# Optimization experiments

Measured on AMD Instinct MI355X. Metric: run time of the kernel, lower is better.

## Reference

```python
import jax, jax.numpy as jnp
import numpy as np

N = 50000      # nodes
E = 800000     # edges in normalized A (incl. self loops)
DIN = 128      # input_dim
DOUT = 64      # output_dim
BN_EPS = 1e-5
SLOPE = 0.01   # LeakyReLU default negative slope


def setup_inputs() -> dict:
    key = jax.random.key(0)
    ks = jax.random.split(key, 10)
    H = jax.random.normal(ks[0], (N, DIN), dtype=jnp.float32)
    rows = jax.random.randint(ks[1], (E,), 0, N, dtype=jnp.int32)
    cols = jax.random.randint(ks[2], (E,), 0, N, dtype=jnp.int32)
    # values of the symmetrically normalized adjacency (precomputed in __init__)
    vals = jax.random.uniform(ks[3], (E,), dtype=jnp.float32)
    # BatchNorm1d params/buffers (eval mode: use running stats)
    gamma = 1.0 + 0.1 * jax.random.normal(ks[4], (DIN,), dtype=jnp.float32)
    beta = 0.1 * jax.random.normal(ks[5], (DIN,), dtype=jnp.float32)
    run_mean = 0.1 * jax.random.normal(ks[6], (DIN,), dtype=jnp.float32)
    run_var = 0.5 + jax.random.uniform(ks[7], (DIN,), dtype=jnp.float32)
    # Linear(input_dim, output_dim)
    W = jax.random.normal(ks[8], (DIN, DOUT), dtype=jnp.float32) / np.sqrt(DIN)
    b = 0.01 * jax.random.normal(ks[9], (DOUT,), dtype=jnp.float32)
    return dict(H=H, rows=rows, cols=cols, vals=vals, gamma=gamma, beta=beta,
                run_mean=run_mean, run_var=run_var, W=W, b=b)


def reference(H, rows, cols, vals, gamma, beta, run_mean, run_var, W, b):
    # F.normalize: L2 row normalization with eps=1e-12
    norm = jnp.maximum(jnp.linalg.norm(H, axis=1, keepdims=True), 1e-12)
    Hn = H / norm
    # BatchNorm1d (eval: running stats); dropout is identity in eval
    scale = gamma * jax.lax.rsqrt(run_var + BN_EPS)
    Hb = (Hn - run_mean) * scale + beta
    # Linear projection [N, DIN] @ [DIN, DOUT]
    X = Hb @ W + b
    # SpMM: out[r] = sum_{e: rows[e]==r} vals[e] * X[cols[e]]
    msgs = vals[:, None] * X[cols]            # [E, DOUT] gather + scale
    out = jax.ops.segment_sum(msgs, rows, num_segments=N)
    # LeakyReLU
    return jnp.where(out >= 0, out, SLOPE * out)
```

## Files before the change

kernel.cpp:

```cpp
#include <hip/hip_runtime.h>
#include <hip/hip_fp16.h>

#define N_NODES 50000
#define E_EDGES 800000
#define DIN 128
#define DOUT 64
#define NBUK 196
#define BUKCAP 4608
#define CHUNK 2048
#define NBLKA 391
#define KXBLK 782
#define ASTRIDE 136

typedef short short8 __attribute__((ext_vector_type(8)));
typedef float f32x4 __attribute__((ext_vector_type(4)));

static __device__ __forceinline__ short f2bf(float f)
{
    union { float f; unsigned u; } x{f};
    const unsigned r = x.u + 0x7FFFu + ((x.u >> 16) & 1u);
    return (short)(r >> 16);
}

union SMemFront {
    struct { short A[64][ASTRIDE]; short B[64][ASTRIDE]; } x;
    struct {
        int lhist[NBUK]; int lstart[NBUK]; int lcur[NBUK]; int gbase[NBUK];
        int scn[256];
        unsigned lbinVC[CHUNK];
        unsigned short lbinBR[CHUNK];
    } a;
};

__global__ __launch_bounds__(256) void k_front(
    const float* __restrict__ H, const float* __restrict__ gamma,
    const float* __restrict__ beta, const float* __restrict__ mean,
    const float* __restrict__ var, const float* __restrict__ W,
    const float* __restrict__ bias, unsigned short* __restrict__ X16,
    const int* __restrict__ rows, const int* __restrict__ cols,
    const float* __restrict__ vals, int* __restrict__ gcursor,
    unsigned* __restrict__ midVC, unsigned char* __restrict__ midR)
{
    __shared__ SMemFront sm;
    const int t = threadIdx.x;

    if (blockIdx.x < NBLKA) {
        const int e0 = blockIdx.x * CHUNK;
        const int nC = min(CHUNK, E_EDGES - e0);

        if (t < NBUK) sm.a.lhist[t] = 0;
        __syncthreads();

        unsigned prVC[8];
        unsigned short prBR[8];
#pragma unroll
        for (int k = 0; k < 8; ++k) {
            const int e = e0 + k * 256 + t;
            if (e < E_EDGES) {
                const int r = rows[e];
                const unsigned hv = __half_as_ushort(__float2half(vals[e]));
                prVC[k] = (hv << 16) | (unsigned)cols[e];
                prBR[k] = (unsigned short)r;
                atomicAdd(&sm.a.lhist[r >> 8], 1);
            } else {
                prBR[k] = 0xFFFFu;
            }
        }
        __syncthreads();

        const int v = (t < NBUK) ? sm.a.lhist[t] : 0;
        sm.a.scn[t] = v;
        __syncthreads();
        for (int o = 1; o < 256; o <<= 1) {
            int u = 0;
            if (t >= o) u = sm.a.scn[t - o];
            __syncthreads();
            sm.a.scn[t] += u;
            __syncthreads();
        }
        if (t < NBUK) {
            const int ex = sm.a.scn[t] - v;
            sm.a.lstart[t] = ex;
            sm.a.lcur[t] = ex;
            sm.a.gbase[t] = t * BUKCAP + (v ? atomicAdd(&gcursor[t], v) : 0);
        }
        __syncthreads();

#pragma unroll
        for (int k = 0; k < 8; ++k) {
            if (prBR[k] != 0xFFFFu) {
                const int bk = prBR[k] >> 8;
                const int pos = atomicAdd(&sm.a.lcur[bk], 1);
                sm.a.lbinVC[pos] = prVC[k];
                sm.a.lbinBR[pos] = prBR[k];
            }
        }
        __syncthreads();

        for (int i = t; i < nC; i += 256) {
            const unsigned short br = sm.a.lbinBR[i];
            const int bk = br >> 8;
            const int g = sm.a.gbase[bk] + (i - sm.a.lstart[bk]);
            if (g < (bk + 1) * BUKCAP) {
                midVC[g] = sm.a.lbinVC[i];
                midR[g] = (unsigned char)(br & 255);
            }
        }
        return;
    }

    const int l = t & 63, wv = t >> 6;
    const int R0 = (blockIdx.x - NBLKA) * 64;

    {
        const int n = t >> 2, koff = (t & 3) * 32;
#pragma unroll
        for (int i = 0; i < 16; ++i) {
            const int k = koff + i * 2;
            const unsigned lo = (unsigned short)f2bf(W[k * DOUT + n]);
            const unsigned hi = (unsigned short)f2bf(W[(k + 1) * DOUT + n]);
            *(unsigned*)&sm.x.B[n][k] = lo | (hi << 16);
        }
    }
    {
        const int rloc = t >> 2, sub = t & 3;
        const int r = R0 + rloc;
        float4 h[8];
        if (r < N_NODES) {
            const float4* hp = (const float4*)(H + (size_t)r * DIN + sub * 32);
#pragma unroll
            for (int i = 0; i < 8; ++i) h[i] = hp[i];
        } else {
#pragma unroll
            for (int i = 0; i < 8; ++i) h[i] = make_float4(0.f, 0.f, 0.f, 0.f);
        }
        float ss = 0.f;
#pragma unroll
        for (int i = 0; i < 8; ++i)
            ss += h[i].x * h[i].x + h[i].y * h[i].y + h[i].z * h[i].z + h[i].w * h[i].w;
        ss += __shfl_xor(ss, 1, 64);
        ss += __shfl_xor(ss, 2, 64);
        const float inv = 1.0f / fmaxf(sqrtf(ss), 1e-12f);

        const float4* gp = (const float4*)(gamma + sub * 32);
        const float4* bp = (const float4*)(beta  + sub * 32);
        const float4* mp = (const float4*)(mean  + sub * 32);
        const float4* vp = (const float4*)(var   + sub * 32);
#pragma unroll
        for (int i = 0; i < 8; ++i) {
            const float4 g4 = gp[i], b4 = bp[i], m4 = mp[i], v4 = vp[i];
            const float s0 = g4.x * rsqrtf(v4.x + 1e-5f);
            const float s1 = g4.y * rsqrtf(v4.y + 1e-5f);
            const float s2 = g4.z * rsqrtf(v4.z + 1e-5f);
            const float s3 = g4.w * rsqrtf(v4.w + 1e-5f);
            const float e0 = h[i].x * inv * s0 + (b4.x - m4.x * s0);
            const float e1 = h[i].y * inv * s1 + (b4.y - m4.y * s1);
            const float e2 = h[i].z * inv * s2 + (b4.z - m4.z * s2);
            const float e3 = h[i].w * inv * s3 + (b4.w - m4.w * s3);
            const unsigned u0 = (unsigned short)f2bf(e0) | ((unsigned)(unsigned short)f2bf(e1) << 16);
            const unsigned u1 = (unsigned short)f2bf(e2) | ((unsigned)(unsigned short)f2bf(e3) << 16);
            *(uint2*)&sm.x.A[rloc][sub * 32 + i * 4] = make_uint2(u0, u1);
        }
    }

    const int ml = l & 15, q = l >> 4;
    f32x4 c0, c1, c2, c3;
    {
        const float b0 = bias[ml],      b1 = bias[16 + ml];
        const float b2 = bias[32 + ml], b3 = bias[48 + ml];
        c0 = f32x4{b0, b0, b0, b0};
        c1 = f32x4{b1, b1, b1, b1};
        c2 = f32x4{b2, b2, b2, b2};
        c3 = f32x4{b3, b3, b3, b3};
    }
    __syncthreads();

#pragma unroll
    for (int k0 = 0; k0 < 4; ++k0) {
        const short8 a  = *(const short8*)&sm.x.A[wv * 16 + ml][k0 * 32 + q * 8];
        const short8 b0 = *(const short8*)&sm.x.B[ml][k0 * 32 + q * 8];
        const short8 b1 = *(const short8*)&sm.x.B[16 + ml][k0 * 32 + q * 8];
        const short8 b2 = *(const short8*)&sm.x.B[32 + ml][k0 * 32 + q * 8];
        const short8 b3 = *(const short8*)&sm.x.B[48 + ml][k0 * 32 + q * 8];
        c0 = __builtin_amdgcn_mfma_f32_16x16x32_bf16(a, b0, c0, 0, 0, 0);
        c1 = __builtin_amdgcn_mfma_f32_16x16x32_bf16(a, b1, c1, 0, 0, 0);
        c2 = __builtin_amdgcn_mfma_f32_16x16x32_bf16(a, b2, c2, 0, 0, 0);
        c3 = __builtin_amdgcn_mfma_f32_16x16x32_bf16(a, b3, c3, 0, 0, 0);
    }

    __syncthreads();
    unsigned short* otile = (unsigned short*)&sm.x.A[0][0];
#pragma unroll
    for (int i = 0; i < 4; ++i) {
        const int r = wv * 16 + q * 4 + i;
        otile[r * 64 + ml]      = __half_as_ushort(__float2half(c0[i]));
        otile[r * 64 + 16 + ml] = __half_as_ushort(__float2half(c1[i]));
        otile[r * 64 + 32 + ml] = __half_as_ushort(__float2half(c2[i]));
        otile[r * 64 + 48 + ml] = __half_as_ushort(__float2half(c3[i]));
    }
    __syncthreads();
#pragma unroll
    for (int rep = 0; rep < 2; ++rep) {
        const int id = rep * 256 + t;
        const int row = id >> 3;
        const int off = (id & 7) * 8;
        if (R0 + row < N_NODES)
            *(uint4*)(X16 + (size_t)(R0 + row) * DOUT + off) =
                *(const uint4*)&otile[row * 64 + off];
    }
}

__global__ __launch_bounds__(512) void k_passB(
    const int* __restrict__ gcursor, const unsigned* __restrict__ midVC,
    const unsigned char* __restrict__ midR, unsigned* __restrict__ ev,
    int* __restrict__ rowS, int* __restrict__ rowE)
{
    __shared__ int lhist[256], scn[256], lcur[256];
    const int t = threadIdx.x;
    const int b = blockIdx.x;
    const int base = b * BUKCAP;
    const int total = min(gcursor[b], BUKCAP);

    if (t < 256) lhist[t] = 0;
    __syncthreads();
    for (int i = t; i < total; i += 512)
        atomicAdd(&lhist[midR[base + i]], 1);
    __syncthreads();

    const int v = (t < 256) ? lhist[t] : 0;
    if (t < 256) scn[t] = v;
    __syncthreads();
    for (int o = 1; o < 256; o <<= 1) {
        int u = 0;
        if (t < 256 && t >= o) u = scn[t - o];
        __syncthreads();
        if (t < 256) scn[t] += u;
        __syncthreads();
    }
    if (t < 256) {
        const int ex = scn[t] - v;
        lcur[t] = ex;
        const int gr = (b << 8) | t;
        if (gr < N_NODES) { rowS[gr] = base + ex; rowE[gr] = base + ex + v; }
    }
    __syncthreads();

    for (int i = t; i < total; i += 512) {
        const int lr = midR[base + i];
        const int pos = atomicAdd(&lcur[lr], 1);
        ev[base + pos] = midVC[base + i];
    }
}

__global__ __launch_bounds__(256) void k_spmm(
    const int* __restrict__ rowS, const int* __restrict__ rowE,
    const unsigned* __restrict__ ev, const unsigned short* __restrict__ X16,
    float* __restrict__ out)
{
    const int lane = threadIdx.x & 63;
    const int sub  = lane & 15;
    const int g4   = lane >> 4;
    const int row  = blockIdx.x * 4 + (threadIdx.x >> 6);
    const int s  = rowS[row];
    const int e2 = rowE[row];
    float a0 = 0.f, a1 = 0.f, a2 = 0.f, a3 = 0.f;
    for (int c = s; c < e2; c += 64) {
        const int idx = c + lane;
        unsigned p = 0;
        if (idx < e2) p = ev[idx];
        const int cnt  = min(e2 - c, 64);
        const int jmax = (cnt + 3) >> 2;
        int j = 0;
        for (; j + 1 < jmax; j += 2) {
            const unsigned u0 = (unsigned)__shfl((int)p, j * 4 + g4,     64);
            const unsigned u1 = (unsigned)__shfl((int)p, j * 4 + 4 + g4, 64);
            const uint2 x0 = *(const uint2*)(X16 + (u0 & 0xFFFFu) * DOUT + sub * 4);
            const uint2 x1 = *(const uint2*)(X16 + (u1 & 0xFFFFu) * DOUT + sub * 4);
            const float v0 = __half2float(__ushort_as_half((unsigned short)(u0 >> 16)));
            const float v1 = __half2float(__ushort_as_half((unsigned short)(u1 >> 16)));
            const float2 f00 = __half22float2(*(const __half2*)&x0.x);
            const float2 f01 = __half22float2(*(const __half2*)&x0.y);
            const float2 f10 = __half22float2(*(const __half2*)&x1.x);
            const float2 f11 = __half22float2(*(const __half2*)&x1.y);
            a0 = fmaf(v0, f00.x, a0); a1 = fmaf(v0, f00.y, a1);
            a2 = fmaf(v0, f01.x, a2); a3 = fmaf(v0, f01.y, a3);
            a0 = fmaf(v1, f10.x, a0); a1 = fmaf(v1, f10.y, a1);
            a2 = fmaf(v1, f11.x, a2); a3 = fmaf(v1, f11.y, a3);
        }
        for (; j < jmax; ++j) {
            const unsigned u = (unsigned)__shfl((int)p, j * 4 + g4, 64);
            const uint2 x = *(const uint2*)(X16 + (u & 0xFFFFu) * DOUT + sub * 4);
            const float v = __half2float(__ushort_as_half((unsigned short)(u >> 16)));
            const float2 f0 = __half22float2(*(const __half2*)&x.x);
            const float2 f1 = __half22float2(*(const __half2*)&x.y);
            a0 = fmaf(v, f0.x, a0); a1 = fmaf(v, f0.y, a1);
            a2 = fmaf(v, f1.x, a2); a3 = fmaf(v, f1.y, a3);
        }
    }
    a0 += __shfl_xor(a0, 16, 64); a1 += __shfl_xor(a1, 16, 64);
    a2 += __shfl_xor(a2, 16, 64); a3 += __shfl_xor(a3, 16, 64);
    a0 += __shfl_xor(a0, 32, 64); a1 += __shfl_xor(a1, 32, 64);
    a2 += __shfl_xor(a2, 32, 64); a3 += __shfl_xor(a3, 32, 64);
    if (g4 == 0) {
        float4 r;
        r.x = (a0 >= 0.f) ? a0 : 0.01f * a0;
        r.y = (a1 >= 0.f) ? a1 : 0.01f * a1;
        r.z = (a2 >= 0.f) ? a2 : 0.01f * a2;
        r.w = (a3 >= 0.f) ? a3 : 0.01f * a3;
        *(float4*)(out + (size_t)row * DOUT + sub * 4) = r;
    }
}

extern "C" void kernel_launch(void* const* d_in, const int* in_sizes, int n_in,
                              void* d_out, int out_size, void* d_ws, size_t ws_size,
                              hipStream_t stream)
{
    const float* H     = (const float*)d_in[0];
    const int*   rows  = (const int*)  d_in[1];
    const int*   cols  = (const int*)  d_in[2];
    const float* vals  = (const float*)d_in[3];
    const float* gamma = (const float*)d_in[4];
    const float* beta  = (const float*)d_in[5];
    const float* mean  = (const float*)d_in[6];
    const float* var   = (const float*)d_in[7];
    const float* W     = (const float*)d_in[8];
    const float* bias  = (const float*)d_in[9];
    float* out = (float*)d_out;

    char* ws = (char*)d_ws;
    unsigned short* X16     = (unsigned short*)(ws);
    int*            gcursor = (int*)          (ws +  6400000);
    unsigned*       midVC   = (unsigned*)     (ws +  6400800);
    unsigned char*  midR    = (unsigned char*)(ws + 10013472);
    unsigned*       ev      = (unsigned*)     (ws + 10916640);
    int*            rowS    = (int*)          (ws + 14529312);
    int*            rowE    = (int*)          (ws + 14730016);

    hipMemsetAsync(gcursor, 0, NBUK * sizeof(int), stream);

    k_front<<<NBLKA + KXBLK, 256, 0, stream>>>(H, gamma, beta, mean, var, W,
                                               bias, X16, rows, cols, vals,
                                               gcursor, midVC, midR);
    k_passB<<<NBUK, 512, 0, stream>>>(gcursor, midVC, midR, ev, rowS, rowE);
    k_spmm<<<N_NODES / 4, 256, 0, stream>>>(rowS, rowE, ev, X16, out);
}
```

Measured before the change: 148.5 us.

## Fuse bucket sort and SpMM into per-bucket LDS atomic accumulation kernel

Replaces the per-bucket counting-sort pass and the CSR row-parallel SpMM with a single kernel that processes each bucket's edges directly, accumulating scaled gathered X rows into a 256x64 fp32 shared-memory tile via LDS atomics, then applies LeakyReLU and writes the output. This removes one kernel launch and the global write/read of the sorted edge array and row pointers. In exchange, it uses only one block per bucket, which lowers parallelism, and it adds shared-memory atomic contention; summation order also becomes nondeterministic.

Result: slower. 470.9 us (+217.1%).

```diff
diff --git a/kernel.cpp b/kernel.cpp
--- a/kernel.cpp
+++ b/kernel.cpp
@@ -11,6 +11,7 @@
 #define NBLKA 391
 #define KXBLK 782
 #define ASTRIDE 136
+#define ACC_STRIDE 68
 
 typedef short short8 __attribute__((ext_vector_type(8)));
 typedef float f32x4 __attribute__((ext_vector_type(4)));
@@ -210,104 +211,77 @@
     }
 }
 
-__global__ __launch_bounds__(512) void k_passB(
+__global__ __launch_bounds__(512) void k_spmm_buk(
     const int* __restrict__ gcursor, const unsigned* __restrict__ midVC,
-    const unsigned char* __restrict__ midR, unsigned* __restrict__ ev,
-    int* __restrict__ rowS, int* __restrict__ rowE)
+    const unsigned char* __restrict__ midR,
+    const unsigned short* __restrict__ X16, float* __restrict__ out)
 {
-    __shared__ int lhist[256], scn[256], lcur[256];
+    __shared__ float acc[256 * ACC_STRIDE];
     const int t = threadIdx.x;
     const int b = blockIdx.x;
     const int base = b * BUKCAP;
     const int total = min(gcursor[b], BUKCAP);
-
-    if (t < 256) lhist[t] = 0;
-    __syncthreads();
-    for (int i = t; i < total; i += 512)
-        atomicAdd(&lhist[midR[base + i]], 1);
-    __syncthreads();
-
-    const int v = (t < 256) ? lhist[t] : 0;
-    if (t < 256) scn[t] = v;
-    __syncthreads();
-    for (int o = 1; o < 256; o <<= 1) {
-        int u = 0;
-        if (t < 256 && t >= o) u = scn[t - o];
-        __syncthreads();
-        if (t < 256) scn[t] += u;
-        __syncthreads();
-    }
-    if (t < 256) {
-        const int ex = scn[t] - v;
-        lcur[t] = ex;
-        const int gr = (b << 8) | t;
-        if (gr < N_NODES) { rowS[gr] = base + ex; rowE[gr] = base + ex + v; }
-    }
-    __syncthreads();
-
-    for (int i = t; i < total; i += 512) {
-        const int lr = midR[base + i];
-        const int pos = atomicAdd(&lcur[lr], 1);
-        ev[base + pos] = midVC[base + i];
-    }
-}
-
-__global__ __launch_bounds__(256) void k_spmm(
-    const int* __restrict__ rowS, const int* __restrict__ rowE,
-    const unsigned* __restrict__ ev, const unsigned short* __restrict__ X16,
-    float* __restrict__ out)
-{
-    const int lane = threadIdx.x & 63;
-    const int sub  = lane & 15;
-    const int g4   = lane >> 4;
-    const int row  = blockIdx.x * 4 + (threadIdx.x >> 6);
-    const int s  = rowS[row];
-    const int e2 = rowE[row];
-    float a0 = 0.f, a1 = 0.f, a2 = 0.f, a3 = 0.f;
-    for (int c = s; c < e2; c += 64) {
-        const int idx = c + lane;
-        unsigned p = 0;
-        if (idx < e2) p = ev[idx];
-        const int cnt  = min(e2 - c, 64);
-        const int jmax = (cnt + 3) >> 2;
-        int j = 0;
-        for (; j + 1 < jmax; j += 2) {
-            const unsigned u0 = (unsigned)__shfl((int)p, j * 4 + g4,     64);
-            const unsigned u1 = (unsigned)__shfl((int)p, j * 4 + 4 + g4, 64);
-            const uint2 x0 = *(const uint2*)(X16 + (u0 & 0xFFFFu) * DOUT + sub * 4);
-            const uint2 x1 = *(const uint2*)(X16 + (u1 & 0xFFFFu) * DOUT + sub * 4);
-            const float v0 = __half2float(__ushort_as_half((unsigned short)(u0 >> 16)));
-            const float v1 = __half2float(__ushort_as_half((unsigned short)(u1 >> 16)));
-            const float2 f00 = __half22float2(*(const __half2*)&x0.x);
-            const float2 f01 = __half22float2(*(const __half2*)&x0.y);
-            const float2 f10 = __half22float2(*(const __half2*)&x1.x);
-            const float2 f11 = __half22float2(*(const __half2*)&x1.y);
-            a0 = fmaf(v0, f00.x, a0); a1 = fmaf(v0, f00.y, a1);
-            a2 = fmaf(v0, f01.x, a2); a3 = fmaf(v0, f01.y, a3);
-            a0 = fmaf(v1, f10.x, a0); a1 = fmaf(v1, f10.y, a1);
-            a2 = fmaf(v1, f11.x, a2); a3 = fmaf(v1, f11.y, a3);
-        }
-        for (; j < jmax; ++j) {
-            const unsigned u = (unsigned)__shfl((int)p, j * 4 + g4, 64);
-            const uint2 x = *(const uint2*)(X16 + (u & 0xFFFFu) * DOUT + sub * 4);
+    const int lane = t & 63;
+    const int wv = t >> 6;
+    const int q = lane >> 3;
+    const int s = lane & 7;
+
+    for (int i = t; i < 256 * ACC_STRIDE / 4; i += 512)
+        *(float4*)&acc[i * 4] = make_float4(0.f, 0.f, 0.f, 0.f);
+    __syncthreads();
+
+    for (int r0 = 0; r0 < total; r0 += 512) {
+        const int idx = base + r0 + t;
+        unsigned vc = 0;
+        int rr = 0;
+        if (r0 + t < total) { vc = midVC[idx]; rr = midR[idx]; }
+        const int n  = min(total - r0 - wv * 64, 64);
+        const int jn = (n + 7) >> 3;
+#pragma unroll 2
+        for (int j = 0; j < jn; ++j) {
+            const int src = (j << 3) | q;
+            const unsigned u = (unsigned)__shfl((int)vc, src, 64);
+            const int r = __shfl(rr, src, 64);
             const float v = __half2float(__ushort_as_half((unsigned short)(u >> 16)));
+            const uint4 x = *(const uint4*)(X16 + (size_t)(u & 0xFFFFu) * DOUT + s * 8);
             const float2 f0 = __half22float2(*(const __half2*)&x.x);
             const float2 f1 = __half22float2(*(const __half2*)&x.y);
-            a0 = fmaf(v, f0.x, a0); a1 = fmaf(v, f0.y, a1);
-            a2 = fmaf(v, f1.x, a2); a3 = fmaf(v, f1.y, a3);
-        }
-    }
-    a0 += __shfl_xor(a0, 16, 64); a1 += __shfl_xor(a1, 16, 64);
-    a2 += __shfl_xor(a2, 16, 64); a3 += __shfl_xor(a3, 16, 64);
-    a0 += __shfl_xor(a0, 32, 64); a1 += __shfl_xor(a1, 32, 64);
-    a2 += __shfl_xor(a2, 32, 64); a3 += __shfl_xor(a3, 32, 64);
-    if (g4 == 0) {
-        float4 r;
-        r.x = (a0 >= 0.f) ? a0 : 0.01f * a0;
-        r.y = (a1 >= 0.f) ? a1 : 0.01f * a1;
-        r.z = (a2 >= 0.f) ? a2 : 0.01f * a2;
-        r.w = (a3 >= 0.f) ? a3 : 0.01f * a3;
-        *(float4*)(out + (size_t)row * DOUT + sub * 4) = r;
+            const float2 f2 = __half22float2(*(const __half2*)&x.z);
+            const float2 f3 = __half22float2(*(const __half2*)&x.w);
+            float* ap = &acc[r * ACC_STRIDE + s];
+            atomicAdd(ap +  0, v * f0.x);
+            atomicAdd(ap +  8, v * f0.y);
+            atomicAdd(ap + 16, v * f1.x);
+            atomicAdd(ap + 24, v * f1.y);
+            atomicAdd(ap + 32, v * f2.x);
+            atomicAdd(ap + 40, v * f2.y);
+            atomicAdd(ap + 48, v * f3.x);
+            atomicAdd(ap + 56, v * f3.y);
+        }
+    }
+    __syncthreads();
+
+    const int gr0 = b << 8;
+#pragma unroll
+    for (int rep = 0; rep < 8; ++rep) {
+        const int id = rep * 512 + t;
+        const int lr = id >> 4;
+        const int m  = id & 15;
+        const int gr = gr0 + lr;
+        if (gr < N_NODES) {
+            float vv[4];
+#pragma unroll
+            for (int i2 = 0; i2 < 4; ++i2) {
+                const int c = m * 4 + i2;
+                vv[i2] = acc[lr * ACC_STRIDE + ((c & 7) << 3) + (c >> 3)];
+            }
+            float4 o;
+            o.x = (vv[0] >= 0.f) ? vv[0] : 0.01f * vv[0];
+            o.y = (vv[1] >= 0.f) ? vv[1] : 0.01f * vv[1];
+            o.z = (vv[2] >= 0.f) ? vv[2] : 0.01f * vv[2];
+            o.w = (vv[3] >= 0.f) ? vv[3] : 0.01f * vv[3];
+            *(float4*)(out + (size_t)gr * DOUT + m * 4) = o;
+        }
     }
 }
 
@@ -332,15 +306,11 @@
     int*            gcursor = (int*)          (ws +  6400000);
     unsigned*       midVC   = (unsigned*)     (ws +  6400800);
     unsigned char*  midR    = (unsigned char*)(ws + 10013472);
-    unsigned*       ev      = (unsigned*)     (ws + 10916640);
-    int*            rowS    = (int*)          (ws + 14529312);
-    int*            rowE    = (int*)          (ws + 14730016);
 
     hipMemsetAsync(gcursor, 0, NBUK * sizeof(int), stream);
 
     k_front<<<NBLKA + KXBLK, 256, 0, stream>>>(H, gamma, beta, mean, var, W,
                                                bias, X16, rows, cols, vals,
                                                gcursor, midVC, midR);
-    k_passB<<<NBUK, 512, 0, stream>>>(gcursor, midVC, midR, ev, rowS, rowE);
-    k_spmm<<<N_NODES / 4, 256, 0, stream>>>(rowS, rowE, ev, X16, out);
+    k_spmm_buk<<<NBUK, 512, 0, stream>>>(gcursor, midVC, midR, X16, out);
 }
```

## Fuse three kernels into one persistent kernel with software grid barriers

Applied to the files above, without the earlier changes.

Merges the front (bucketing plus projection), bucket-sort and SpMM kernels into one persistent kernel of 768 blocks separated by atomic grid barriers. The dense projection now overlaps with the bucket-sort pass instead of running with the bucketing phase. The aim is to remove kernel launch overhead and the idle tail between kernels. In exchange it relies on all 768 blocks being co-resident (launch_bounds 256,4) to avoid deadlock, and gives up some parallelism and occupancy because work now runs in grid-stride loops.

After: 448.2 us. +201.8%, slower.

```diff
diff --git a/kernel.cpp b/kernel.cpp
--- a/kernel.cpp
+++ b/kernel.cpp
@@ -11,6 +11,7 @@
 #define NBLKA 391
 #define KXBLK 782
 #define ASTRIDE 136
+#define GRID 768
 
 typedef short short8 __attribute__((ext_vector_type(8)));
 typedef float f32x4 __attribute__((ext_vector_type(4)));
@@ -22,7 +23,7 @@
     return (short)(r >> 16);
 }
 
-union SMemFront {
+union SMemAll {
     struct { short A[64][ASTRIDE]; short B[64][ASTRIDE]; } x;
     struct {
         int lhist[NBUK]; int lstart[NBUK]; int lcur[NBUK]; int gbase[NBUK];
@@ -30,18 +31,32 @@
         unsigned lbinVC[CHUNK];
         unsigned short lbinBR[CHUNK];
     } a;
+    struct { int lhist[256]; int scn[256]; int lcur[256]; } b;
 };
 
-__global__ __launch_bounds__(256) void k_front(
+static __device__ __forceinline__ void grid_barrier(int* bar)
+{
+    __syncthreads();
+    if (threadIdx.x == 0) {
+        __hip_atomic_fetch_add(bar, 1, __ATOMIC_ACQ_REL, __HIP_MEMORY_SCOPE_AGENT);
+        while (__hip_atomic_load(bar, __ATOMIC_ACQUIRE, __HIP_MEMORY_SCOPE_AGENT) < GRID)
+            __builtin_amdgcn_s_sleep(1);
+    }
+    __syncthreads();
+}
+
+__global__ __launch_bounds__(256, 4) void k_all(
     const float* __restrict__ H, const float* __restrict__ gamma,
     const float* __restrict__ beta, const float* __restrict__ mean,
     const float* __restrict__ var, const float* __restrict__ W,
-    const float* __restrict__ bias, unsigned short* __restrict__ X16,
-    const int* __restrict__ rows, const int* __restrict__ cols,
-    const float* __restrict__ vals, int* __restrict__ gcursor,
-    unsigned* __restrict__ midVC, unsigned char* __restrict__ midR)
+    const float* __restrict__ bias, const int* __restrict__ rows,
+    const int* __restrict__ cols, const float* __restrict__ vals,
+    unsigned short* __restrict__ X16, int* __restrict__ gcursor,
+    int* __restrict__ bar, unsigned* __restrict__ midVC,
+    unsigned char* __restrict__ midR, unsigned* __restrict__ ev,
+    int* __restrict__ rowS, int* __restrict__ rowE, float* __restrict__ out)
 {
-    __shared__ SMemFront sm;
+    __shared__ SMemAll sm;
     const int t = threadIdx.x;
 
     if (blockIdx.x < NBLKA) {
@@ -106,208 +121,204 @@
                 midR[g] = (unsigned char)(br & 255);
             }
         }
-        return;
     }
-
-    const int l = t & 63, wv = t >> 6;
-    const int R0 = (blockIdx.x - NBLKA) * 64;
+    grid_barrier(&bar[0]);
+
+    if (blockIdx.x < NBUK) {
+        const int b = blockIdx.x;
+        const int base = b * BUKCAP;
+        const int total = min(gcursor[b], BUKCAP);
+
+        sm.b.lhist[t] = 0;
+        __syncthreads();
+        for (int i = t; i < total; i += 256)
+            atomicAdd(&sm.b.lhist[midR[base + i]], 1);
+        __syncthreads();
+
+        const int v = sm.b.lhist[t];
+        sm.b.scn[t] = v;
+        __syncthreads();
+        for (int o = 1; o < 256; o <<= 1) {
+            int u = 0;
+            if (t >= o) u = sm.b.scn[t - o];
+            __syncthreads();
+            sm.b.scn[t] += u;
+            __syncthreads();
+        }
+        {
+            const int ex = sm.b.scn[t] - v;
+            sm.b.lcur[t] = ex;
+            const int gr = (b << 8) | t;
+            if (gr < N_NODES) { rowS[gr] = base + ex; rowE[gr] = base + ex + v; }
+        }
+        __syncthreads();
+
+        for (int i = t; i < total; i += 256) {
+            const int lr = midR[base + i];
+            const int pos = atomicAdd(&sm.b.lcur[lr], 1);
+            ev[base + pos] = midVC[base + i];
+        }
+    } else {
+        for (int u = blockIdx.x - NBUK; u < KXBLK; u += GRID - NBUK) {
+            const int l = t & 63, wvx = t >> 6;
+            const int R0 = u * 64;
+
+            {
+                const int n = t >> 2, koff = (t & 3) * 32;
+#pragma unroll
+                for (int i = 0; i < 16; ++i) {
+                    const int k = koff + i * 2;
+                    const unsigned lo = (unsigned short)f2bf(W[k * DOUT + n]);
+                    const unsigned hi = (unsigned short)f2bf(W[(k + 1) * DOUT + n]);
+                    *(unsigned*)&sm.x.B[n][k] = lo | (hi << 16);
+                }
+            }
+            {
+                const int rloc = t >> 2, sub = t & 3;
+                const int r = R0 + rloc;
+                float4 h[8];
+                if (r < N_NODES) {
+                    const float4* hp = (const float4*)(H + (size_t)r * DIN + sub * 32);
+#pragma unroll
+                    for (int i = 0; i < 8; ++i) h[i] = hp[i];
+                } else {
+#pragma unroll
+                    for (int i = 0; i < 8; ++i) h[i] = make_float4(0.f, 0.f, 0.f, 0.f);
+                }
+                float ss = 0.f;
+#pragma unroll
+                for (int i = 0; i < 8; ++i)
+                    ss += h[i].x * h[i].x + h[i].y * h[i].y + h[i].z * h[i].z + h[i].w * h[i].w;
+                ss += __shfl_xor(ss, 1, 64);
+                ss += __shfl_xor(ss, 2, 64);
+                const float inv = 1.0f / fmaxf(sqrtf(ss), 1e-12f);
+
+                const float4* gp = (const float4*)(gamma + sub * 32);
+                const float4* bp = (const float4*)(beta  + sub * 32);
+                const float4* mp = (const float4*)(mean  + sub * 32);
+                const float4* vp = (const float4*)(var   + sub * 32);
+#pragma unroll
+                for (int i = 0; i < 8; ++i) {
+                    const float4 g4 = gp[i], b4 = bp[i], m4 = mp[i], v4 = vp[i];
+                    const float s0 = g4.x * rsqrtf(v4.x + 1e-5f);
+                    const float s1 = g4.y * rsqrtf(v4.y + 1e-5f);
+                    const float s2 = g4.z * rsqrtf(v4.z + 1e-5f);
+                    const float s3 = g4.w * rsqrtf(v4.w + 1e-5f);
+                    const float e0 = h[i].x * inv * s0 + (b4.x - m4.x * s0);
+                    const float e1 = h[i].y * inv * s1 + (b4.y - m4.y * s1);
+                    const float e2 = h[i].z * inv * s2 + (b4.z - m4.z * s2);
+                    const float e3 = h[i].w * inv * s3 + (b4.w - m4.w * s3);
+                    const unsigned u0 = (unsigned short)f2bf(e0) | ((unsigned)(unsigned short)f2bf(e1) << 16);
+                    const unsigned u1 = (unsigned short)f2bf(e2) | ((unsigned)(unsigned short)f2bf(e3) << 16);
+                    *(uint2*)&sm.x.A[rloc][sub * 32 + i * 4] = make_uint2(u0, u1);
+                }
+            }
+
+            const int ml = l & 15, q = l >> 4;
+            f32x4 c0, c1, c2, c3;
+            {
+                const float b0 = bias[ml],      b1 = bias[16 + ml];
+                const float b2 = bias[32 + ml], b3 = bias[48 + ml];
+                c0 = f32x4{b0, b0, b0, b0};
+                c1 = f32x4{b1, b1, b1, b1};
+                c2 = f32x4{b2, b2, b2, b2};
+                c3 = f32x4{b3, b3, b3, b3};
+            }
+            __syncthreads();
+
+#pragma unroll
+            for (int k0 = 0; k0 < 4; ++k0) {
+                const short8 a  = *(const short8*)&sm.x.A[wvx * 16 + ml][k0 * 32 + q * 8];
+                const short8 b0 = *(const short8*)&sm.x.B[ml][k0 * 32 + q * 8];
+                const short8 b1 = *(const short8*)&sm.x.B[16 + ml][k0 * 32 + q * 8];
+                const short8 b2 = *(const short8*)&sm.x.B[32 + ml][k0 * 32 + q * 8];
+                const short8 b3 = *(const short8*)&sm.x.B[48 + ml][k0 * 32 + q * 8];
+                c0 = __builtin_amdgcn_mfma_f32_16x16x32_bf16(a, b0, c0, 0, 0, 0);
+                c1 = __builtin_amdgcn_mfma_f32_16x16x32_bf16(a, b1, c1, 0, 0, 0);
+                c2 = __builtin_amdgcn_mfma_f32_16x16x32_bf16(a, b2, c2, 0, 0, 0);
+                c3 = __builtin_amdgcn_mfma_f32_16x16x32_bf16(a, b3, c3, 0, 0, 0);
+            }
+
+            __syncthreads();
+            unsigned short* otile = (unsigned short*)&sm.x.A[0][0];
+#pragma unroll
+            for (int i = 0; i < 4; ++i) {
+                const int r = wvx * 16 + q * 4 + i;
+                otile[r * 64 + ml]      = __half_as_ushort(__float2half(c0[i]));
+                otile[r * 64 + 16 + ml] = __half_as_ushort(__float2half(c1[i]));
+                otile[r * 64 + 32 + ml] = __half_as_ushort(__float2half(c2[i]));
+                otile[r * 64 + 48 + ml] = __half_as_ushort(__float2half(c3[i]));
+            }
+            __syncthreads();
+#pragma unroll
+            for (int rep = 0; rep < 2; ++rep) {
+                const int id = rep * 256 + t;
+                const int row = id >> 3;
+                const int off = (id & 7) * 8;
+                if (R0 + row < N_NODES)
+                    *(uint4*)(X16 + (size_t)(R0 + row) * DOUT + off) =
+                        *(const uint4*)&otile[row * 64 + off];
+            }
+            __syncthreads();
+        }
+    }
+    grid_barrier(&bar[1]);
 
     {
-        const int n = t >> 2, koff = (t & 3) * 32;
-#pragma unroll
-        for (int i = 0; i < 16; ++i) {
-            const int k = koff + i * 2;
-            const unsigned lo = (unsigned short)f2bf(W[k * DOUT + n]);
-            const unsigned hi = (unsigned short)f2bf(W[(k + 1) * DOUT + n]);
-            *(unsigned*)&sm.x.B[n][k] = lo | (hi << 16);
-        }
-    }
-    {
-        const int rloc = t >> 2, sub = t & 3;
-        const int r = R0 + rloc;
-        float4 h[8];
-        if (r < N_NODES) {
-            const float4* hp = (const float4*)(H + (size_t)r * DIN + sub * 32);
-#pragma unroll
-            for (int i = 0; i < 8; ++i) h[i] = hp[i];
-        } else {
-#pragma unroll
-            for (int i = 0; i < 8; ++i) h[i] = make_float4(0.f, 0.f, 0.f, 0.f);
-        }
-        float ss = 0.f;
-#pragma unroll
-        for (int i = 0; i < 8; ++i)
-            ss += h[i].x * h[i].x + h[i].y * h[i].y + h[i].z * h[i].z + h[i].w * h[i].w;
-        ss += __shfl_xor(ss, 1, 64);
-        ss += __shfl_xor(ss, 2, 64);
-        const float inv = 1.0f / fmaxf(sqrtf(ss), 1e-12f);
-
-        const float4* gp = (const float4*)(gamma + sub * 32);
-        const float4* bp = (const float4*)(beta  + sub * 32);
-        const float4* mp = (const float4*)(mean  + sub * 32);
-        const float4* vp = (const float4*)(var   + sub * 32);
-#pragma unroll
-        for (int i = 0; i < 8; ++i) {
-            const float4 g4 = gp[i], b4 = bp[i], m4 = mp[i], v4 = vp[i];
-            const float s0 = g4.x * rsqrtf(v4.x + 1e-5f);
-            const float s1 = g4.y * rsqrtf(v4.y + 1e-5f);
-            const float s2 = g4.z * rsqrtf(v4.z + 1e-5f);
-            const float s3 = g4.w * rsqrtf(v4.w + 1e-5f);
-            const float e0 = h[i].x * inv * s0 + (b4.x - m4.x * s0);
-            const float e1 = h[i].y * inv * s1 + (b4.y - m4.y * s1);
-            const float e2 = h[i].z * inv * s2 + (b4.z - m4.z * s2);
-            const float e3 = h[i].w * inv * s3 + (b4.w - m4.w * s3);
-            const unsigned u0 = (unsigned short)f2bf(e0) | ((unsigned)(unsigned short)f2bf(e1) << 16);
-            const unsigned u1 = (unsigned short)f2bf(e2) | ((unsigned)(unsigned short)f2bf(e3) << 16);
-            *(uint2*)&sm.x.A[rloc][sub * 32 + i * 4] = make_uint2(u0, u1);
-        }
-    }
-
-    const int ml = l & 15, q = l >> 4;
-    f32x4 c0, c1, c2, c3;
-    {
-        const float b0 = bias[ml],      b1 = bias[16 + ml];
-        const float b2 = bias[32 + ml], b3 = bias[48 + ml];
-        c0 = f32x4{b0, b0, b0, b0};
-        c1 = f32x4{b1, b1, b1, b1};
-        c2 = f32x4{b2, b2, b2, b2};
-        c3 = f32x4{b3, b3, b3, b3};
-    }
-    __syncthreads();
-
-#pragma unroll
-    for (int k0 = 0; k0 < 4; ++k0) {
-        const short8 a  = *(const short8*)&sm.x.A[wv * 16 + ml][k0 * 32 + q * 8];
-        const short8 b0 = *(const short8*)&sm.x.B[ml][k0 * 32 + q * 8];
-        const short8 b1 = *(const short8*)&sm.x.B[16 + ml][k0 * 32 + q * 8];
-        const short8 b2 = *(const short8*)&sm.x.B[32 + ml][k0 * 32 + q * 8];
-        const short8 b3 = *(const short8*)&sm.x.B[48 + ml][k0 * 32 + q * 8];
-        c0 = __builtin_amdgcn_mfma_f32_16x16x32_bf16(a, b0, c0, 0, 0, 0);
-        c1 = __builtin_amdgcn_mfma_f32_16x16x32_bf16(a, b1, c1, 0, 0, 0);
-        c2 = __builtin_amdgcn_mfma_f32_16x16x32_bf16(a, b2, c2, 0, 0, 0);
-        c3 = __builtin_amdgcn_mfma_f32_16x16x32_bf16(a, b3, c3, 0, 0, 0);
-    }
-
-    __syncthreads();
-    unsigned short* otile = (unsigned short*)&sm.x.A[0][0];
-#pragma unroll
-    for (int i = 0; i < 4; ++i) {
-        const int r = wv * 16 + q * 4 + i;
-        otile[r * 64 + ml]      = __half_as_ushort(__float2half(c0[i]));
-        otile[r * 64 + 16 + ml] = __half_as_ushort(__float2half(c1[i]));
-        otile[r * 64 + 32 + ml] = __half_as_ushort(__float2half(c2[i]));
-        otile[r * 64 + 48 + ml] = __half_as_ushort(__float2half(c3[i]));
-    }
-    __syncthreads();
-#pragma unroll
-    for (int rep = 0; rep < 2; ++rep) {
-        const int id = rep * 256 + t;
-        const int row = id >> 3;
-        const int off = (id & 7) * 8;
-        if (R0 + row < N_NODES)
-            *(uint4*)(X16 + (size_t)(R0 + row) * DOUT + off) =
-                *(const uint4*)&otile[row * 64 + off];
-    }
-}
-
-__global__ __launch_bounds__(512) void k_passB(
-    const int* __restrict__ gcursor, const unsigned* __restrict__ midVC,
-    const unsigned char* __restrict__ midR, unsigned* __restrict__ ev,
-    int* __restrict__ rowS, int* __restrict__ rowE)
-{
-    __shared__ int lhist[256], scn[256], lcur[256];
-    const int t = threadIdx.x;
-    const int b = blockIdx.x;
-    const int base = b * BUKCAP;
-    const int total = min(gcursor[b], BUKCAP);
-
-    if (t < 256) lhist[t] = 0;
-    __syncthreads();
-    for (int i = t; i < total; i += 512)
-        atomicAdd(&lhist[midR[base + i]], 1);
-    __syncthreads();
-
-    const int v = (t < 256) ? lhist[t] : 0;
-    if (t < 256) scn[t] = v;
-    __syncthreads();
-    for (int o = 1; o < 256; o <<= 1) {
-        int u = 0;
-        if (t < 256 && t >= o) u = scn[t - o];
-        __syncthreads();
-        if (t < 256) scn[t] += u;
-        __syncthreads();
-    }
-    if (t < 256) {
-        const int ex = scn[t] - v;
-        lcur[t] = ex;
-        const int gr = (b << 8) | t;
-        if (gr < N_NODES) { rowS[gr] = base + ex; rowE[gr] = base + ex + v; }
-    }
-    __syncthreads();
-
-    for (int i = t; i < total; i += 512) {
-        const int lr = midR[base + i];
-        const int pos = atomicAdd(&lcur[lr], 1);
-        ev[base + pos] = midVC[base + i];
-    }
-}
-
-__global__ __launch_bounds__(256) void k_spmm(
-    const int* __restrict__ rowS, const int* __restrict__ rowE,
-    const unsigned* __restrict__ ev, const unsigned short* __restrict__ X16,
-    float* __restrict__ out)
-{
-    const int lane = threadIdx.x & 63;
-    const int sub  = lane & 15;
-    const int g4   = lane >> 4;
-    const int row  = blockIdx.x * 4 + (threadIdx.x >> 6);
-    const int s  = rowS[row];
-    const int e2 = rowE[row];
-    float a0 = 0.f, a1 = 0.f, a2 = 0.f, a3 = 0.f;
-    for (int c = s; c < e2; c += 64) {
-        const int idx = c + lane;
-        unsigned p = 0;
-        if (idx < e2) p = ev[idx];
-        const int cnt  = min(e2 - c, 64);
-        const int jmax = (cnt + 3) >> 2;
-        int j = 0;
-        for (; j + 1 < jmax; j += 2) {
-            const unsigned u0 = (unsigned)__shfl((int)p, j * 4 + g4,     64);
-            const unsigned u1 = (unsigned)__shfl((int)p, j * 4 + 4 + g4, 64);
-            const uint2 x0 = *(const uint2*)(X16 + (u0 & 0xFFFFu) * DOUT + sub * 4);
-            const uint2 x1 = *(const uint2*)(X16 + (u1 & 0xFFFFu) * DOUT + sub * 4);
-            const float v0 = __half2float(__ushort_as_half((unsigned short)(u0 >> 16)));
-            const float v1 = __half2float(__ushort_as_half((unsigned short)(u1 >> 16)));
-            const float2 f00 = __half22float2(*(const __half2*)&x0.x);
-            const float2 f01 = __half22float2(*(const __half2*)&x0.y);
-            const float2 f10 = __half22float2(*(const __half2*)&x1.x);
-            const float2 f11 = __half22float2(*(const __half2*)&x1.y);
-            a0 = fmaf(v0, f00.x, a0); a1 = fmaf(v0, f00.y, a1);
-            a2 = fmaf(v0, f01.x, a2); a3 = fmaf(v0, f01.y, a3);
-            a0 = fmaf(v1, f10.x, a0); a1 = fmaf(v1, f10.y, a1);
-            a2 = fmaf(v1, f11.x, a2); a3 = fmaf(v1, f11.y, a3);
-        }
-        for (; j < jmax; ++j) {
-            const unsigned u = (unsigned)__shfl((int)p, j * 4 + g4, 64);
-            const uint2 x = *(const uint2*)(X16 + (u & 0xFFFFu) * DOUT + sub * 4);
-            const float v = __half2float(__ushort_as_half((unsigned short)(u >> 16)));
-            const float2 f0 = __half22float2(*(const __half2*)&x.x);
-            const float2 f1 = __half22float2(*(const __half2*)&x.y);
-            a0 = fmaf(v, f0.x, a0); a1 = fmaf(v, f0.y, a1);
-            a2 = fmaf(v, f1.x, a2); a3 = fmaf(v, f1.y, a3);
-        }
-    }
-    a0 += __shfl_xor(a0, 16, 64); a1 += __shfl_xor(a1, 16, 64);
-    a2 += __shfl_xor(a2, 16, 64); a3 += __shfl_xor(a3, 16, 64);
-    a0 += __shfl_xor(a0, 32, 64); a1 += __shfl_xor(a1, 32, 64);
-    a2 += __shfl_xor(a2, 32, 64); a3 += __shfl_xor(a3, 32, 64);
-    if (g4 == 0) {
-        float4 r;
-        r.x = (a0 >= 0.f) ? a0 : 0.01f * a0;
-        r.y = (a1 >= 0.f) ? a1 : 0.01f * a1;
-        r.z = (a2 >= 0.f) ? a2 : 0.01f * a2;
-        r.w = (a3 >= 0.f) ? a3 : 0.01f * a3;
-        *(float4*)(out + (size_t)row * DOUT + sub * 4) = r;
+        const int lane = threadIdx.x & 63;
+        const int sub  = lane & 15;
+        const int g4   = lane >> 4;
+        for (int g = blockIdx.x; g < N_NODES / 4; g += GRID) {
+            const int row = g * 4 + (t >> 6);
+            const int s  = rowS[row];
+            const int e2 = rowE[row];
+            float a0 = 0.f, a1 = 0.f, a2 = 0.f, a3 = 0.f;
+            for (int c = s; c < e2; c += 64) {
+                const int idx = c + lane;
+                unsigned p = 0;
+                if (idx < e2) p = ev[idx];
+                const int cnt  = min(e2 - c, 64);
+                const int jmax = (cnt + 3) >> 2;
+                int j = 0;
+                for (; j + 1 < jmax; j += 2) {
+                    const unsigned u0 = (unsigned)__shfl((int)p, j * 4 + g4,     64);
+                    const unsigned u1 = (unsigned)__shfl((int)p, j * 4 + 4 + g4, 64);
+                    const uint2 x0 = *(const uint2*)(X16 + (u0 & 0xFFFFu) * DOUT + sub * 4);
+                    const uint2 x1 = *(const uint2*)(X16 + (u1 & 0xFFFFu) * DOUT + sub * 4);
+                    const float v0 = __half2float(__ushort_as_half((unsigned short)(u0 >> 16)));
+                    const float v1 = __half2float(__ushort_as_half((unsigned short)(u1 >> 16)));
+                    const float2 f00 = __half22float2(*(const __half2*)&x0.x);
+                    const float2 f01 = __half22float2(*(const __half2*)&x0.y);
+                    const float2 f10 = __half22float2(*(const __half2*)&x1.x);
+                    const float2 f11 = __half22float2(*(const __half2*)&x1.y);
+                    a0 = fmaf(v0, f00.x, a0); a1 = fmaf(v0, f00.y, a1);
+                    a2 = fmaf(v0, f01.x, a2); a3 = fmaf(v0, f01.y, a3);
+                    a0 = fmaf(v1, f10.x, a0); a1 = fmaf(v1, f10.y, a1);
+                    a2 = fmaf(v1, f11.x, a2); a3 = fmaf(v1, f11.y, a3);
+                }
+                for (; j < jmax; ++j) {
+                    const unsigned u = (unsigned)__shfl((int)p, j * 4 + g4, 64);
+                    const uint2 x = *(const uint2*)(X16 + (u & 0xFFFFu) * DOUT + sub * 4);
+                    const float v = __half2float(__ushort_as_half((unsigned short)(u >> 16)));
+                    const float2 f0 = __half22float2(*(const __half2*)&x.x);
+                    const float2 f1 = __half22float2(*(const __half2*)&x.y);
+                    a0 = fmaf(v, f0.x, a0); a1 = fmaf(v, f0.y, a1);
+                    a2 = fmaf(v, f1.x, a2); a3 = fmaf(v, f1.y, a3);
+                }
+            }
+            a0 += __shfl_xor(a0, 16, 64); a1 += __shfl_xor(a1, 16, 64);
+            a2 += __shfl_xor(a2, 16, 64); a3 += __shfl_xor(a3, 16, 64);
+            a0 += __shfl_xor(a0, 32, 64); a1 += __shfl_xor(a1, 32, 64);
+            a2 += __shfl_xor(a2, 32, 64); a3 += __shfl_xor(a3, 32, 64);
+            if (g4 == 0) {
+                float4 r;
+                r.x = (a0 >= 0.f) ? a0 : 0.01f * a0;
+                r.y = (a1 >= 0.f) ? a1 : 0.01f * a1;
+                r.z = (a2 >= 0.f) ? a2 : 0.01f * a2;
+                r.w = (a3 >= 0.f) ? a3 : 0.01f * a3;
+                *(float4*)(out + (size_t)row * DOUT + sub * 4) = r;
+            }
+        }
     }
 }
 
@@ -330,17 +341,16 @@
     char* ws = (char*)d_ws;
     unsigned short* X16     = (unsigned short*)(ws);
     int*            gcursor = (int*)          (ws +  6400000);
+    int*            bar     = (int*)          (ws +  6400784);
     unsigned*       midVC   = (unsigned*)     (ws +  6400800);
     unsigned char*  midR    = (unsigned char*)(ws + 10013472);
     unsigned*       ev      = (unsigned*)     (ws + 10916640);
     int*            rowS    = (int*)          (ws + 14529312);
     int*            rowE    = (int*)          (ws + 14730016);
 
-    hipMemsetAsync(gcursor, 0, NBUK * sizeof(int), stream);
-
-    k_front<<<NBLKA + KXBLK, 256, 0, stream>>>(H, gamma, beta, mean, var, W,
-                                               bias, X16, rows, cols, vals,
-                                               gcursor, midVC, midR);
-    k_passB<<<NBUK, 512, 0, stream>>>(gcursor, midVC, midR, ev, rowS, rowE);
-    k_spmm<<<N_NODES / 4, 256, 0, stream>>>(rowS, rowE, ev, X16, out);
+    hipMemsetAsync(gcursor, 0, 800, stream);
+
+    k_all<<<GRID, 256, 0, stream>>>(H, gamma, beta, mean, var, W, bias,
+                                    rows, cols, vals, X16, gcursor, bar,
+                                    midVC, midR, ev, rowS, rowE, out);
 }
```
